# Kernel tuning notes

Hardware: AMD Instinct MI355X
Metric: run time of the kernel (lower is better)

The kernel has to match this reference:

```python
import jax, jax.numpy as jnp
import numpy as np

N, E, H = 50000, 800000, 128
HQ = H // 4  # 32


def _mlp(x, w1, b1, w2, b2):
    return jax.nn.relu(x @ w1 + b1) @ w2 + b2


def setup_inputs() -> dict:
    key = jax.random.key(0)
    ks = jax.random.split(key, 16)

    def lin(k, fan_in, fan_out):
        lim = 1.0 / np.sqrt(fan_in)
        kw, kb = jax.random.split(k)
        w = jax.random.uniform(kw, (fan_in, fan_out), jnp.float32, -lim, lim)
        b = jax.random.uniform(kb, (fan_out,), jnp.float32, -lim, lim)
        return w, b

    x = jax.random.normal(ks[0], (N, H), jnp.float32)
    pos = jax.random.normal(ks[1], (N, 3), jnp.float32)
    edge_index = jax.random.randint(ks[2], (2, E), 0, N, jnp.int64)

    pw1, pb1 = lin(ks[3], 3, HQ)
    pw2, pb2 = lin(ks[4], HQ, HQ)
    mw1, mb1 = lin(ks[5], 2 * H + HQ, H)
    mw2, mb2 = lin(ks[6], H, H)
    uw1, ub1 = lin(ks[7], 2 * H, H)
    uw2, ub2 = lin(ks[8], H, H)

    return dict(x=x, pos=pos, edge_index=edge_index,
                pw1=pw1, pb1=pb1, pw2=pw2, pb2=pb2,
                mw1=mw1, mb1=mb1, mw2=mw2, mb2=mb2,
                uw1=uw1, ub1=ub1, uw2=uw2, ub2=ub2)


def reference(x, pos, edge_index,
              pw1, pb1, pw2, pb2,
              mw1, mb1, mw2, mb2,
              uw1, ub1, uw2, ub2):
    row, col = edge_index[0], edge_index[1]
    # position features from relative positions [E, 3] -> [E, H//4]
    pos_feat = _mlp(pos[row] - pos[col], pw1, pb1, pw2, pb2)
    # per-edge messages [E, 2H + H//4] -> [E, H]
    msg_in = jnp.concatenate([x[row], x[col], pos_feat], axis=-1)
    messages = _mlp(msg_in, mw1, mb1, mw2, mb2)
    # scatter-add messages into destination nodes (index_add on col)
    agg = jax.ops.segment_sum(messages, col, num_segments=x.shape[0])
    # node update [N, 2H] -> [N, H]
    return _mlp(jnp.concatenate([x, agg], axis=-1), uw1, ub1, uw2, ub2)
```

## Files before the change

kernel.cpp:

```cpp
#include <hip/hip_runtime.h>
#include <hip/hip_bf16.h>

#define NN 50000
#define NE 800000
#define HD 128
#define SCAN_CHUNK 1024
#define SCAN_BLOCKS ((NN + SCAN_CHUNK - 1) / SCAN_CHUNK)
#define NB_NODE 1024
#define EPB ((NE + NB_NODE - 1) / NB_NODE)
#define NB_SCAT ((NE / 2 + 255) / 256)

typedef __attribute__((ext_vector_type(8))) short s16x8;
typedef __attribute__((ext_vector_type(4))) float f32x4;

static __device__ __forceinline__ unsigned short f2bf(float f) {
    unsigned int u = __float_as_uint(f);
    u = (u + 0x7FFFu + ((u >> 16) & 1u)) >> 16;
    return (unsigned short)u;
}
static __device__ __forceinline__ float bf2f(unsigned short h) {
    return __uint_as_float(((unsigned int)h) << 16);
}
static __device__ __forceinline__ unsigned int f2bf2(float lo, float hi) {
    __hip_bfloat162 h = __float22bfloat162_rn(make_float2(lo, hi));
    return *reinterpret_cast<unsigned int*>(&h);
}

#define WFENCE() do { asm volatile("s_waitcnt lgkmcnt(0)" ::: "memory"); \
                      __builtin_amdgcn_sched_barrier(0); } while (0)

__global__ __launch_bounds__(256, 3) void node_kernel(
    const float* __restrict__ x, const float* __restrict__ mw1,
    const float* __restrict__ mb1, const float* __restrict__ pb2,
    const int* __restrict__ ei,
    unsigned short* __restrict__ xa, unsigned short* __restrict__ xb,
    float* __restrict__ aggH, int* __restrict__ cnt)
{
    __shared__ __align__(16) unsigned short sB[128 * 136];
    __shared__ __align__(16) unsigned short sSt[4][16 * 132];
    __shared__ int sIdx64;

    int bid = blockIdx.x;
    int tid = threadIdx.x;

    {
        f32x4 z = {0.f, 0.f, 0.f, 0.f};
        const int total4 = NN * HD / 4;
        for (int i = bid * 256 + tid; i < total4; i += NB_NODE * 256)
            ((f32x4*)aggH)[i] = z;
    }
    if (tid == 0) {
        int z = 1;
        for (int k = 0; k < 16; ++k) if (ei[2 * k + 1] != 0) z = 0;
        sIdx64 = z;
    }
    int half = bid & 1;
    for (int idx = tid; idx < 128 * 128; idx += 256) {
        int c = idx & 127, k = idx >> 7;
        sB[c * 136 + k] = f2bf(mw1[(half * 128 + k) * 128 + c]);
    }
    __syncthreads();

    {
        int he0 = bid * EPB;
        int he1 = he0 + EPB; if (he1 > NE) he1 = NE;
        if (sIdx64) {
            for (int e = he0 + tid; e < he1; e += 256)
                atomicAdd(&cnt[ei[2 * NE + 2 * e]], 1);
        } else {
            for (int e = he0 + tid; e < he1; e += 256)
                atomicAdd(&cnt[ei[NE + e]], 1);
        }
    }

    int lane = tid & 63, wv = tid >> 6;
    int r16 = lane & 15, g4 = lane >> 4;
    unsigned short* st = sSt[wv];
    unsigned short* dst = half ? xb : xa;

    float bcr[8];
    #pragma unroll
    for (int tc = 0; tc < 8; ++tc) bcr[tc] = 0.f;
    if (half) {
        #pragma unroll
        for (int tc = 0; tc < 8; ++tc) bcr[tc] = mb1[tc * 16 + r16];
        for (int i = 0; i < 32; ++i) {
            float pv = pb2[i];
            #pragma unroll
            for (int tc = 0; tc < 8; ++tc)
                bcr[tc] = fmaf(pv, mw1[(256 + i) * 128 + tc * 16 + r16], bcr[tc]);
        }
    }

    const int NT = NN / 16;
    const int nb = NB_NODE >> 1;
    const int nbid = bid >> 1;

    for (int t = nbid * 4 + wv; t < NT; t += nb * 4) {
        int r0 = t * 16;
        int row = r0 + r16;
        s16x8 a[4];
        #pragma unroll
        for (int ks = 0; ks < 4; ++ks) {
            const float* p = &x[(size_t)row * HD + ks * 32 + g4 * 8];
            float4 v0 = *(const float4*)p;
            float4 v1 = *(const float4*)(p + 4);
            union { s16x8 v; unsigned int u[4]; } av;
            av.u[0] = f2bf2(v0.x, v0.y); av.u[1] = f2bf2(v0.z, v0.w);
            av.u[2] = f2bf2(v1.x, v1.y); av.u[3] = f2bf2(v1.z, v1.w);
            a[ks] = av.v;
        }
        float hold[4];
        #pragma unroll
        for (int tc = 0; tc < 8; ++tc) {
            int col = tc * 16 + r16;
            float bv = bcr[tc];
            f32x4 acc = {bv, bv, bv, bv};
            #pragma unroll
            for (int ks = 0; ks < 4; ++ks) {
                s16x8 b = *(const s16x8*)&sB[col * 136 + ks * 32 + g4 * 8];
                acc = __builtin_amdgcn_mfma_f32_16x16x32_bf16(a[ks], b, acc, 0, 0, 0);
            }
            if ((tc & 1) == 0) {
                #pragma unroll
                for (int j = 0; j < 4; ++j) hold[j] = acc[j];
            } else {
                #pragma unroll
                for (int j = 0; j < 4; ++j)
                    *(unsigned int*)&st[(g4 * 4 + j) * 132 + r16 * 8 + (tc - 1)] =
                        f2bf2(hold[j], acc[j]);
            }
        }
        WFENCE();
        #pragma unroll
        for (int i = 0; i < 4; ++i) {
            int idx = i * 512 + lane * 8;
            int rr = idx >> 7, cc = idx & 127;
            *(s16x8*)&dst[(size_t)(r0 + rr) * HD + cc] = *(const s16x8*)&st[rr * 132 + cc];
        }
        WFENCE();
    }
}

__global__ void scan1_kernel(const int* __restrict__ cnt, int* __restrict__ cursor,
                             int* __restrict__ bsum)
{
    __shared__ int tot[256];
    int b = blockIdx.x, t = threadIdx.x;
    int i0 = b * SCAN_CHUNK + t * 4;
    int v[4];
    #pragma unroll
    for (int k = 0; k < 4; ++k) v[k] = (i0 + k < NN) ? cnt[i0 + k] : 0;
    tot[t] = v[0] + v[1] + v[2] + v[3];
    __syncthreads();
    if (t == 0) {
        int run = 0;
        for (int i = 0; i < 256; ++i) { int x = tot[i]; tot[i] = run; run += x; }
        bsum[b] = run;
    }
    __syncthreads();
    int p = tot[t];
    #pragma unroll
    for (int k = 0; k < 4; ++k) {
        if (i0 + k < NN) cursor[i0 + k] = p;
        p += v[k];
    }
}

__global__ void scan3_kernel(int* __restrict__ cursor, const int* __restrict__ bsum)
{
    __shared__ int sCarry;
    int b = blockIdx.x, t = threadIdx.x;
    if (t == 0) {
        int run = 0;
        for (int i = 0; i < b; ++i) run += bsum[i];
        sCarry = run;
    }
    __syncthreads();
    int carry = sCarry;
    int i0 = b * SCAN_CHUNK + t * 4;
    #pragma unroll
    for (int k = 0; k < 4; ++k)
        if (i0 + k < NN) cursor[i0 + k] += carry;
}

__global__ void scatterprep_kernel(
    const int* __restrict__ ei, int* __restrict__ cursor, int2* __restrict__ sRC,
    const float* __restrict__ pw2, const float* __restrict__ mw1,
    const float* __restrict__ mw2, const float* __restrict__ mb2,
    const float* __restrict__ uw1,
    float* __restrict__ Wpc, float* __restrict__ W3, float* __restrict__ b3)
{
    __shared__ int sIdx64;
    int bid = blockIdx.x, tid = threadIdx.x;

    if (bid >= NB_SCAT) {
        int rb = bid - NB_SCAT;
        if (rb == 64) {
            for (int idx = tid; idx < 32 * 128; idx += 256) {
                int j = idx >> 7, k = idx & 127;
                float s = 0.f;
                #pragma unroll 8
                for (int i = 0; i < 32; ++i) s += pw2[j * 32 + i] * mw1[(256 + i) * 128 + k];
                Wpc[idx] = s;
            }
            return;
        }
        int idx = rb * 256 + tid;
        {
            int k = idx >> 7, j = idx & 127;
            float s = 0.f;
            #pragma unroll 4
            for (int c = 0; c < 128; ++c)
                s += mw2[k * 128 + c] * uw1[(128 + c) * 128 + j];
            W3[idx] = s;
        }
        if (rb == 0 && tid < 128) {
            int j = tid;
            float s = 0.f;
            #pragma unroll 4
            for (int c = 0; c < 128; ++c)
                s += mb2[c] * uw1[(128 + c) * 128 + j];
            b3[j] = s;
        }
        return;
    }

    if (tid == 0) {
        int z = 1;
        for (int k = 0; k < 16; ++k) if (ei[2 * k + 1] != 0) z = 0;
        sIdx64 = z;
    }
    __syncthreads();
    int g = bid * 256 + tid;
    if (g >= NE / 2) return;
    int e0 = g * 2;
    int r0, r1, c0, c1;
    if (sIdx64) {
        int4 qr = *(const int4*)&ei[2 * e0];           r0 = qr.x; r1 = qr.z;
        int4 qc = *(const int4*)&ei[2 * NE + 2 * e0];  c0 = qc.x; c1 = qc.z;
    } else {
        int2 qr = *(const int2*)&ei[e0];       r0 = qr.x; r1 = qr.y;
        int2 qc = *(const int2*)&ei[NE + e0];  c0 = qc.x; c1 = qc.y;
    }
    int p0 = atomicAdd(&cursor[c0], 1);
    sRC[p0] = make_int2(r0, c0);
    int p1 = atomicAdd(&cursor[c1], 1);
    sRC[p1] = make_int2(r1, c1);
}

__global__ __launch_bounds__(256, 3) void edge_kernel(
    const float* __restrict__ pos, const int2* __restrict__ sRC,
    const float* __restrict__ pw1, const float* __restrict__ pb1,
    const unsigned short* __restrict__ xa, const unsigned short* __restrict__ xb,
    const float* __restrict__ Wpc,
    float* __restrict__ aggH)
{
    __shared__ __align__(16) unsigned short sT[4][16 * 136];
    __shared__ int sECs[4][16];

    int tid = threadIdx.x;
    int lane = tid & 63, wv = tid >> 6;
    int r16 = lane & 15, g4 = lane >> 4;
    unsigned short* stg = sT[wv];
    int* secw = sECs[wv];

    s16x8 wr[8];
    #pragma unroll
    for (int tc = 0; tc < 8; ++tc) {
        s16x8 w;
        #pragma unroll
        for (int i = 0; i < 8; ++i)
            w[i] = (short)f2bf(Wpc[(g4 * 8 + i) * 128 + tc * 16 + r16]);
        wr[tc] = w;
    }
    float pw10[8], pw11[8], pw12[8], pb1r[8];
    #pragma unroll
    for (int i = 0; i < 8; ++i) {
        int k = g4 * 8 + i;
        pw10[i] = pw1[k]; pw11[i] = pw1[32 + k]; pw12[i] = pw1[64 + k];
        pb1r[i] = pb1[k];
    }

    const int NW = gridDim.x * 4;
    const int NT = NE / 16;
    int gw = blockIdx.x * 4 + wv;
    if (gw >= NT) return;

    int2 rc = sRC[gw * 16 + r16];
    int2 rcN = rc;
    if (gw + NW < NT) rcN = sRC[(gw + NW) * 16 + r16];
    float dp0 = pos[rc.x * 3 + 0] - pos[rc.y * 3 + 0];
    float dp1 = pos[rc.x * 3 + 1] - pos[rc.y * 3 + 1];
    float dp2 = pos[rc.x * 3 + 2] - pos[rc.y * 3 + 2];
    s16x8 ga[4], gb[4];
    #pragma unroll
    for (int j = 0; j < 4; ++j) {
        int gx = __shfl(rc.x, g4 * 4 + j, 64);
        int gy = __shfl(rc.y, g4 * 4 + j, 64);
        ga[j] = *(const s16x8*)&xa[(size_t)gx * HD + r16 * 8];
        gb[j] = *(const s16x8*)&xb[(size_t)gy * HD + r16 * 8];
    }

    for (int t = gw; t < NT; t += NW) {
        bool hn  = (t + NW) < NT;
        bool hn2 = (t + 2 * NW) < NT;

        if (lane < 16) secw[lane] = rc.y;
        union { s16x8 v; unsigned int u[4]; } apf;
        #pragma unroll
        for (int i2 = 0; i2 < 4; ++i2) {
            int i = 2 * i2;
            float v0 = fmaf(dp0, pw10[i], fmaf(dp1, pw11[i], fmaf(dp2, pw12[i], pb1r[i])));
            float v1 = fmaf(dp0, pw10[i+1], fmaf(dp1, pw11[i+1], fmaf(dp2, pw12[i+1], pb1r[i+1])));
            apf.u[i2] = f2bf2(fmaxf(v0, 0.f), fmaxf(v1, 0.f));
        }

        float hold[4];
        #pragma unroll
        for (int tc = 0; tc < 8; ++tc) {
            f32x4 acc;
            #pragma unroll
            for (int j = 0; j < 4; ++j)
                acc[j] = bf2f((unsigned short)ga[j][tc]) + bf2f((unsigned short)gb[j][tc]);
            acc = __builtin_amdgcn_mfma_f32_16x16x32_bf16(apf.v, wr[tc], acc, 0, 0, 0);
            if ((tc & 1) == 0) {
                #pragma unroll
                for (int j = 0; j < 4; ++j) hold[j] = fmaxf(acc[j], 0.f);
            } else {
                #pragma unroll
                for (int j = 0; j < 4; ++j)
                    *(unsigned int*)&stg[(g4 * 4 + j) * 136 + r16 * 8 + (tc - 1)] =
                        f2bf2(hold[j], fmaxf(acc[j], 0.f));
            }
        }
        WFENCE();

        if (hn) {
            #pragma unroll
            for (int j = 0; j < 4; ++j) {
                int gx = __shfl(rcN.x, g4 * 4 + j, 64);
                int gy = __shfl(rcN.y, g4 * 4 + j, 64);
                ga[j] = *(const s16x8*)&xa[(size_t)gx * HD + r16 * 8];
                gb[j] = *(const s16x8*)&xb[(size_t)gy * HD + r16 * 8];
            }
        }

        int2 rcN2 = rcN;
        if (hn2) rcN2 = sRC[(t + 2 * NW) * 16 + r16];
        float dp0N = 0.f, dp1N = 0.f, dp2N = 0.f;
        if (hn) {
            dp0N = pos[rcN.x * 3 + 0] - pos[rcN.y * 3 + 0];
            dp1N = pos[rcN.x * 3 + 1] - pos[rcN.y * 3 + 1];
            dp2N = pos[rcN.x * 3 + 2] - pos[rcN.y * 3 + 2];
        }

        {
            int p0 = (lane & 15) * 8 + (lane >> 4);
            int p1 = p0 + 4;
            int cur = secw[0];
            float run0 = bf2f(stg[p0]);
            float run1 = bf2f(stg[p1]);
            #pragma unroll
            for (int e = 1; e < 16; ++e) {
                int c = secw[e];
                float v0 = bf2f(stg[e * 136 + p0]);
                float v1 = bf2f(stg[e * 136 + p1]);
                if (c != cur) {
                    unsafeAtomicAdd(&aggH[(size_t)cur * HD + lane], run0);
                    unsafeAtomicAdd(&aggH[(size_t)cur * HD + lane + 64], run1);
                    cur = c; run0 = v0; run1 = v1;
                } else { run0 += v0; run1 += v1; }
            }
            unsafeAtomicAdd(&aggH[(size_t)cur * HD + lane], run0);
            unsafeAtomicAdd(&aggH[(size_t)cur * HD + lane + 64], run1);
        }
        WFENCE();

        rc = rcN; rcN = rcN2; dp0 = dp0N; dp1 = dp1N; dp2 = dp2N;
    }
}

__global__ __launch_bounds__(768, 1) void upd_kernel(
    const float* __restrict__ x, const float* __restrict__ aggH,
    const int* __restrict__ cnt,
    const float* __restrict__ uw1, const float* __restrict__ ub1,
    const float* __restrict__ W3, const float* __restrict__ b3,
    const float* __restrict__ uw2, const float* __restrict__ ub2,
    float* __restrict__ out)
{
    __shared__ __align__(16) unsigned short sB1a[128 * 136];
    __shared__ __align__(16) unsigned short sW3l[128 * 136];
    __shared__ __align__(16) unsigned short sB2[128 * 136];
    __shared__ __align__(16) unsigned short sSt[12][16 * 136];

    int tid = threadIdx.x;
    for (int idx = tid; idx < 128 * 128; idx += 768) {
        int c = idx & 127, k = idx >> 7;
        sB1a[c * 136 + k] = f2bf(uw1[k * 128 + c]);
        sW3l[c * 136 + k] = f2bf(W3[k * 128 + c]);
        sB2[c * 136 + k]  = f2bf(uw2[k * 128 + c]);
    }
    __syncthreads();

    int lane = tid & 63, wv = tid >> 6;
    int r16 = lane & 15, g4 = lane >> 4;
    unsigned short* st = sSt[wv];
    float ub1r[8], ub2r[8], b3r[8];
    #pragma unroll
    for (int tc = 0; tc < 8; ++tc) {
        ub1r[tc] = ub1[tc * 16 + r16];
        ub2r[tc] = ub2[tc * 16 + r16];
        b3r[tc]  = b3[tc * 16 + r16];
    }

    const int NT = NN / 16;
    for (int t = blockIdx.x * 12 + wv; t < NT; t += gridDim.x * 12) {
        int r0 = t * 16;
        int row = r0 + r16;
        s16x8 a[8];
        #pragma unroll
        for (int ks = 0; ks < 8; ++ks) {
            const float* p = (ks < 4) ? &x[(size_t)row * HD + ks * 32 + g4 * 8]
                                      : &aggH[(size_t)row * HD + (ks - 4) * 32 + g4 * 8];
            float4 v0 = *(const float4*)p;
            float4 v1 = *(const float4*)(p + 4);
            union { s16x8 v; unsigned int u[4]; } av;
            av.u[0] = f2bf2(v0.x, v0.y); av.u[1] = f2bf2(v0.z, v0.w);
            av.u[2] = f2bf2(v1.x, v1.y); av.u[3] = f2bf2(v1.z, v1.w);
            a[ks] = av.v;
        }
        float cn[4];
        #pragma unroll
        for (int j = 0; j < 4; ++j) cn[j] = (float)cnt[r0 + g4 * 4 + j];

        #pragma unroll
        for (int tc = 0; tc < 8; ++tc) {
            int col = tc * 16 + r16;
            f32x4 acc;
            #pragma unroll
            for (int j = 0; j < 4; ++j) acc[j] = ub1r[tc] + cn[j] * b3r[tc];
            #pragma unroll
            for (int ks = 0; ks < 4; ++ks) {
                s16x8 b = *(const s16x8*)&sB1a[col * 136 + ks * 32 + g4 * 8];
                acc = __builtin_amdgcn_mfma_f32_16x16x32_bf16(a[ks], b, acc, 0, 0, 0);
            }
            #pragma unroll
            for (int ks = 4; ks < 8; ++ks) {
                s16x8 b = *(const s16x8*)&sW3l[col * 136 + (ks - 4) * 32 + g4 * 8];
                acc = __builtin_amdgcn_mfma_f32_16x16x32_bf16(a[ks], b, acc, 0, 0, 0);
            }
            #pragma unroll
            for (int j = 0; j < 4; ++j)
                st[(g4 * 4 + j) * 136 + col] = f2bf(fmaxf(acc[j], 0.f));
        }
        WFENCE();
        s16x8 a2[4];
        #pragma unroll
        for (int ks = 0; ks < 4; ++ks)
            a2[ks] = *(const s16x8*)&st[r16 * 136 + ks * 32 + g4 * 8];
        WFENCE();
        #pragma unroll
        for (int tc = 0; tc < 8; ++tc) {
            int col = tc * 16 + r16;
            float bv = ub2r[tc];
            f32x4 acc = {bv, bv, bv, bv};
            #pragma unroll
            for (int ks = 0; ks < 4; ++ks) {
                s16x8 b = *(const s16x8*)&sB2[col * 136 + ks * 32 + g4 * 8];
                acc = __builtin_amdgcn_mfma_f32_16x16x32_bf16(a2[ks], b, acc, 0, 0, 0);
            }
            #pragma unroll
            for (int j = 0; j < 4; ++j)
                out[(size_t)(r0 + g4 * 4 + j) * HD + col] = acc[j];
        }
    }
}

extern "C" void kernel_launch(void* const* d_in, const int* in_sizes, int n_in,
                              void* d_out, int out_size, void* d_ws, size_t ws_size,
                              hipStream_t stream)
{
    const float* x   = (const float*)d_in[0];
    const float* pos = (const float*)d_in[1];
    const int*   ei  = (const int*)d_in[2];
    const float* pw1 = (const float*)d_in[3];
    const float* pb1 = (const float*)d_in[4];
    const float* pw2 = (const float*)d_in[5];
    const float* pb2 = (const float*)d_in[6];
    const float* mw1 = (const float*)d_in[7];
    const float* mb1 = (const float*)d_in[8];
    const float* mw2 = (const float*)d_in[9];
    const float* mb2 = (const float*)d_in[10];
    const float* uw1 = (const float*)d_in[11];
    const float* ub1 = (const float*)d_in[12];
    const float* uw2 = (const float*)d_in[13];
    const float* ub2 = (const float*)d_in[14];
    float* out = (float*)d_out;

    char* ws = (char*)d_ws;
    float*          aggH   = (float*)(ws);
    unsigned short* xa     = (unsigned short*)(ws + 25600000);
    unsigned short* xb     = (unsigned short*)(ws + 38400000);
    float*          Wpc    = (float*)(ws + 51200000);
    int*            cnt    = (int*)(ws + 51216896);
    int*            cursor = (int*)(ws + 51417600);
    int*            bsum   = (int*)(ws + 51618304);
    int2*           sRC    = (int2*)(ws + 51618560);
    float*          W3     = (float*)(ws + 58018560);
    float*          b3     = (float*)(ws + 58084096);

    hipMemsetAsync(cnt, 0, NN * sizeof(int), stream);
    node_kernel<<<NB_NODE, 256, 0, stream>>>(x, mw1, mb1, pb2, ei, xa, xb, aggH, cnt);
    scan1_kernel<<<SCAN_BLOCKS, 256, 0, stream>>>(cnt, cursor, bsum);
    scan3_kernel<<<SCAN_BLOCKS, 256, 0, stream>>>(cursor, bsum);
    scatterprep_kernel<<<NB_SCAT + 65, 256, 0, stream>>>(
        ei, cursor, sRC, pw2, mw1, mw2, mb2, uw1, Wpc, W3, b3);
    edge_kernel<<<768, 256, 0, stream>>>(pos, sRC, pw1, pb1, xa, xb, Wpc, aggH);
    upd_kernel<<<256, 768, 0, stream>>>(x, aggH, cnt, uw1, ub1, W3, b3, uw2, ub2, out);
}
```

Before: 215.9 us.

## Split sorted edge array into row and column arrays, fill columns during scan

The sorted edge list changes from interleaved (row,col) int2 pairs to separate row and column int arrays. The column array is filled directly in the scan kernel by writing each node id into its CSR segment, so the atomic scatter only writes the row index. In the edge kernel, the per-wave LDS staging of destination ids is replaced by wave-uniform loads from the column array. This cuts scatter write traffic and an LDS round trip, but adds a serial per-node fill loop in the scan kernel whose length depends on node degree.

```diff
diff --git a/kernel.cpp b/kernel.cpp
--- a/kernel.cpp
+++ b/kernel.cpp
@@ -167,7 +167,8 @@
     }
 }
 
-__global__ void scan3_kernel(int* __restrict__ cursor, const int* __restrict__ bsum)
+__global__ void scan3_kernel(int* __restrict__ cursor, const int* __restrict__ bsum,
+                             const int* __restrict__ cnt, int* __restrict__ sC)
 {
     __shared__ int sCarry;
     int b = blockIdx.x, t = threadIdx.x;
@@ -180,12 +181,19 @@
     int carry = sCarry;
     int i0 = b * SCAN_CHUNK + t * 4;
     #pragma unroll
-    for (int k = 0; k < 4; ++k)
-        if (i0 + k < NN) cursor[i0 + k] += carry;
+    for (int k = 0; k < 4; ++k) {
+        int i = i0 + k;
+        if (i < NN) {
+            int s = cursor[i] + carry;
+            cursor[i] = s;
+            int n = cnt[i];
+            for (int j = 0; j < n; ++j) sC[s + j] = i;
+        }
+    }
 }
 
 __global__ void scatterprep_kernel(
-    const int* __restrict__ ei, int* __restrict__ cursor, int2* __restrict__ sRC,
+    const int* __restrict__ ei, int* __restrict__ cursor, int* __restrict__ sR,
     const float* __restrict__ pw2, const float* __restrict__ mw1,
     const float* __restrict__ mw2, const float* __restrict__ mb2,
     const float* __restrict__ uw1,
@@ -244,26 +252,25 @@
         int2 qc = *(const int2*)&ei[NE + e0];  c0 = qc.x; c1 = qc.y;
     }
     int p0 = atomicAdd(&cursor[c0], 1);
-    sRC[p0] = make_int2(r0, c0);
+    sR[p0] = r0;
     int p1 = atomicAdd(&cursor[c1], 1);
-    sRC[p1] = make_int2(r1, c1);
+    sR[p1] = r1;
 }
 
 __global__ __launch_bounds__(256, 3) void edge_kernel(
-    const float* __restrict__ pos, const int2* __restrict__ sRC,
+    const float* __restrict__ pos,
+    const int* __restrict__ sR, const int* __restrict__ sC,
     const float* __restrict__ pw1, const float* __restrict__ pb1,
     const unsigned short* __restrict__ xa, const unsigned short* __restrict__ xb,
     const float* __restrict__ Wpc,
     float* __restrict__ aggH)
 {
     __shared__ __align__(16) unsigned short sT[4][16 * 136];
-    __shared__ int sECs[4][16];
 
     int tid = threadIdx.x;
     int lane = tid & 63, wv = tid >> 6;
     int r16 = lane & 15, g4 = lane >> 4;
     unsigned short* stg = sT[wv];
-    int* secw = sECs[wv];
 
     s16x8 wr[8];
     #pragma unroll
@@ -287,9 +294,14 @@
     int gw = blockIdx.x * 4 + wv;
     if (gw >= NT) return;
 
-    int2 rc = sRC[gw * 16 + r16];
-    int2 rcN = rc;
-    if (gw + NW < NT) rcN = sRC[(gw + NW) * 16 + r16];
+    int2 rc, rcN;
+    rc.x = sR[gw * 16 + r16];
+    rc.y = sC[gw * 16 + r16];
+    rcN = rc;
+    if (gw + NW < NT) {
+        rcN.x = sR[(gw + NW) * 16 + r16];
+        rcN.y = sC[(gw + NW) * 16 + r16];
+    }
     float dp0 = pos[rc.x * 3 + 0] - pos[rc.y * 3 + 0];
     float dp1 = pos[rc.x * 3 + 1] - pos[rc.y * 3 + 1];
     float dp2 = pos[rc.x * 3 + 2] - pos[rc.y * 3 + 2];
@@ -306,7 +318,6 @@
         bool hn  = (t + NW) < NT;
         bool hn2 = (t + 2 * NW) < NT;
 
-        if (lane < 16) secw[lane] = rc.y;
         union { s16x8 v; unsigned int u[4]; } apf;
         #pragma unroll
         for (int i2 = 0; i2 < 4; ++i2) {
@@ -347,7 +358,11 @@
         }
 
         int2 rcN2 = rcN;
-        if (hn2) rcN2 = sRC[(t + 2 * NW) * 16 + r16];
+        if (hn2) {
+            int i2x = (t + 2 * NW) * 16 + r16;
+            rcN2.x = sR[i2x];
+            rcN2.y = sC[i2x];
+        }
         float dp0N = 0.f, dp1N = 0.f, dp2N = 0.f;
         if (hn) {
             dp0N = pos[rcN.x * 3 + 0] - pos[rcN.y * 3 + 0];
@@ -356,14 +371,16 @@
         }
 
         {
+            int tb = __builtin_amdgcn_readfirstlane(t);
+            const int* __restrict__ scp = sC + tb * 16;
             int p0 = (lane & 15) * 8 + (lane >> 4);
             int p1 = p0 + 4;
-            int cur = secw[0];
+            int cur = scp[0];
             float run0 = bf2f(stg[p0]);
             float run1 = bf2f(stg[p1]);
             #pragma unroll
             for (int e = 1; e < 16; ++e) {
-                int c = secw[e];
+                int c = scp[e];
                 float v0 = bf2f(stg[e * 136 + p0]);
                 float v1 = bf2f(stg[e * 136 + p1]);
                 if (c != cur) {
@@ -506,16 +523,17 @@
     int*            cnt    = (int*)(ws + 51216896);
     int*            cursor = (int*)(ws + 51417600);
     int*            bsum   = (int*)(ws + 51618304);
-    int2*           sRC    = (int2*)(ws + 51618560);
+    int*            sR     = (int*)(ws + 51618560);
+    int*            sC     = (int*)(ws + 54818560);
     float*          W3     = (float*)(ws + 58018560);
     float*          b3     = (float*)(ws + 58084096);
 
     hipMemsetAsync(cnt, 0, NN * sizeof(int), stream);
     node_kernel<<<NB_NODE, 256, 0, stream>>>(x, mw1, mb1, pb2, ei, xa, xb, aggH, cnt);
     scan1_kernel<<<SCAN_BLOCKS, 256, 0, stream>>>(cnt, cursor, bsum);
-    scan3_kernel<<<SCAN_BLOCKS, 256, 0, stream>>>(cursor, bsum);
+    scan3_kernel<<<SCAN_BLOCKS, 256, 0, stream>>>(cursor, bsum, cnt, sC);
     scatterprep_kernel<<<NB_SCAT + 65, 256, 0, stream>>>(
-        ei, cursor, sRC, pw2, mw1, mw2, mb2, uw1, Wpc, W3, b3);
-    edge_kernel<<<768, 256, 0, stream>>>(pos, sRC, pw1, pb1, xa, xb, Wpc, aggH);
+        ei, cursor, sR, pw2, mw1, mw2, mb2, uw1, Wpc, W3, b3);
+    edge_kernel<<<768, 256, 0, stream>>>(pos, sR, sC, pw1, pb1, xa, xb, Wpc, aggH);
     upd_kernel<<<256, 768, 0, stream>>>(x, aggH, cnt, uw1, ub1, W3, b3, uw2, ub2, out);
 }
```

Result: no change. 215.3 us (-0.3%).
